# Kernel optimization log

Hardware: AMD Instinct MI355X
Metric: run time of the kernel (lower is better)

## Reference

```python
import jax, jax.numpy as jnp
import numpy as np

B, T, D, E, H = 4, 2048, 1024, 8, 1024  # H = hidden_units // num_experts


def setup_inputs() -> dict:
    key = jax.random.key(0)
    ks = jax.random.split(key, 5)
    s = 0.02
    return {
        "x": jax.random.normal(ks[0], (B, T, D), dtype=jnp.float32),
        "Wp": jax.random.normal(ks[1], (D, E), dtype=jnp.float32) * s,
        "bp": jnp.zeros((E,), dtype=jnp.float32),
        "W1": jax.random.normal(ks[2], (E, D, H), dtype=jnp.float32) * s,
        "b1": jnp.zeros((E, H), dtype=jnp.float32),
        "W2": jax.random.normal(ks[3], (E, H, D), dtype=jnp.float32) * s,
        "b2": jnp.zeros((E, D), dtype=jnp.float32),
    }


def reference(x, Wp, bp, W1, b1, W2, b2):
    b, t, d = x.shape
    e = Wp.shape[1]
    xf = x.reshape(-1, d)                       # [N, D]
    logits = xf @ Wp + bp                       # [N, E]
    probs = jax.nn.softmax(logits, axis=-1)     # [N, E]
    expert_chosen = jnp.argmax(probs, axis=-1)  # top-1 routing, [N]
    expert_probs = jnp.take_along_axis(probs, expert_chosen[:, None], axis=-1)  # [N,1]

    # Dense masked dispatch/combine (same math as gather-FFN-scatter; ReLU FFN,
    # dropout_rate=0 so dropout is identity).
    out = jnp.zeros_like(xf)
    for i in range(e):
        h = jax.nn.relu(xf @ W1[i] + b1[i])     # [N, H]
        y = h @ W2[i] + b2[i]                   # [N, D]
        mask = (expert_chosen == i).astype(xf.dtype)[:, None]
        out = out + mask * y

    # probs / probs.detach() == 1 in forward; gradient-routing trick preserved.
    out = out * (expert_probs / jax.lax.stop_gradient(expert_probs))
    return out.reshape(b, t, d), probs.reshape(b, t, e), expert_chosen.reshape(b, t)
```

## Files before the change

kernel.cpp:

```cpp
#include <hip/hip_runtime.h>
#include <stdint.h>

#define N_TOK 8192
#define D_DIM 1024
#define E_NUM 8

typedef float f32x4 __attribute__((ext_vector_type(4)));
typedef __bf16 bf16x8 __attribute__((ext_vector_type(8)));

__device__ __forceinline__ unsigned short f32_to_bf16_bits(float f) {
  union { float f; uint32_t u; } v; v.f = f;
  uint32_t u = v.u;
  uint32_t r = u + 0x7fffu + ((u >> 16) & 1u);
  return (unsigned short)(r >> 16);
}

__device__ __forceinline__ void load_lds16(const void* g, void* l) {
  __builtin_amdgcn_global_load_lds(
      (const __attribute__((address_space(1))) void*)g,
      (__attribute__((address_space(3))) void*)l, 16, 0, 0);
}

__device__ __forceinline__ void transpose_tile(unsigned short (*T)[72],
                                               const float* __restrict__ S,
                                               unsigned short* __restrict__ O,
                                               int r0, int c0, int t) {
  const int rr = t >> 4;
  const int cc = (t & 15) * 4;
#pragma unroll
  for (int p = 0; p < 4; p++) {
    int r = p * 16 + rr;
    float4 v = *reinterpret_cast<const float4*>(S + (size_t)(r0 + r) * 1024 + c0 + cc);
    T[cc + 0][r] = f32_to_bf16_bits(v.x);
    T[cc + 1][r] = f32_to_bf16_bits(v.y);
    T[cc + 2][r] = f32_to_bf16_bits(v.z);
    T[cc + 3][r] = f32_to_bf16_bits(v.w);
  }
  __syncthreads();
#pragma unroll
  for (int p = 0; p < 4; p++) {
    int c = p * 16 + rr;
    ushort4 o = *reinterpret_cast<const ushort4*>(&T[c][cc]);
    *reinterpret_cast<ushort4*>(O + (size_t)(c0 + c) * 1024 + r0 + cc) = o;
  }
}

__global__ __launch_bounds__(256) void wpt_kernel(const float* __restrict__ Wp,
                                                  float* __restrict__ WpT) {
  int i = blockIdx.x * 256 + threadIdx.x;
  int e = i >> 10, d = i & 1023;
  WpT[i] = Wp[(size_t)d * E_NUM + e];
}

__global__ __launch_bounds__(256) void routing_w1t_kernel(
    const float* __restrict__ x, const float* __restrict__ WpT,
    const float* __restrict__ bp, float* __restrict__ probs_out,
    float* __restrict__ chosenF, int* __restrict__ chosen,
    unsigned short* __restrict__ xb,
    const float* __restrict__ W1, unsigned short* __restrict__ W1t) {
  __shared__ __align__(16) unsigned short T[64][72];
  __shared__ __align__(16) float pbuf[4][8];
  if (blockIdx.x >= 2048) {
    const int tb = blockIdx.x - 2048;
    const int e = tb >> 8, rc = tb & 255;
    transpose_tile(T, W1 + ((size_t)e << 20), W1t + ((size_t)e << 20),
                   (rc >> 4) * 64, (rc & 15) * 64, threadIdx.x);
    return;
  }
  const int wave = threadIdx.x >> 6;
  const int lane = threadIdx.x & 63;
  const int token = blockIdx.x * 4 + wave;
  const float* xr = x + (size_t)token * D_DIM;
  unsigned short* xbr = xb + (size_t)token * D_DIM;
  double acc[E_NUM];
#pragma unroll
  for (int e = 0; e < E_NUM; e++) acc[e] = 0.0;
#pragma unroll
  for (int it = 0; it < 4; it++) {
    const int d0 = it * 256 + lane * 4;
    float4 xv = *reinterpret_cast<const float4*>(xr + d0);
    ushort4 o;
    o.x = f32_to_bf16_bits(xv.x);
    o.y = f32_to_bf16_bits(xv.y);
    o.z = f32_to_bf16_bits(xv.z);
    o.w = f32_to_bf16_bits(xv.w);
    *reinterpret_cast<ushort4*>(xbr + d0) = o;
#pragma unroll
    for (int e = 0; e < E_NUM; e++) {
      float4 w = *reinterpret_cast<const float4*>(WpT + (e << 10) + d0);
      acc[e] += (double)xv.x * (double)w.x;
      acc[e] += (double)xv.y * (double)w.y;
      acc[e] += (double)xv.z * (double)w.z;
      acc[e] += (double)xv.w * (double)w.w;
    }
  }
#pragma unroll
  for (int e = 0; e < E_NUM; e++) {
#pragma unroll
    for (int off = 32; off > 0; off >>= 1) acc[e] += __shfl_xor(acc[e], off);
  }
  if (lane == 0) {
    double lg[E_NUM];
#pragma unroll
    for (int e = 0; e < E_NUM; e++) lg[e] = acc[e] + (double)bp[e];
    int best = 0;
    double bv = lg[0];
#pragma unroll
    for (int e = 1; e < E_NUM; e++)
      if (lg[e] > bv) { bv = lg[e]; best = e; }
    double s = 0.0, ex[E_NUM];
#pragma unroll
    for (int e = 0; e < E_NUM; e++) { ex[e] = exp(lg[e] - bv); s += ex[e]; }
    double inv = 1.0 / s;
#pragma unroll
    for (int e = 0; e < E_NUM; e++) pbuf[wave][e] = (float)(ex[e] * inv);
    chosenF[token] = (float)best;
    chosen[token] = best;
  }
  __syncthreads();
  if (threadIdx.x < 8) {
    float4 v = *reinterpret_cast<const float4*>(
        &pbuf[threadIdx.x >> 1][(threadIdx.x & 1) * 4]);
    reinterpret_cast<float4*>(probs_out + (size_t)blockIdx.x * 32)[threadIdx.x] = v;
  }
}

__global__ __launch_bounds__(1024) void scan_scatter_kernel(
    const int* __restrict__ chosen, int* __restrict__ offsets,
    int* __restrict__ perm) {
  __shared__ int hist[E_NUM];
  __shared__ int curs[E_NUM];
  const int t = threadIdx.x;
  if (t < E_NUM) hist[t] = 0;
  __syncthreads();
  for (int n = t; n < N_TOK; n += 1024) atomicAdd(&hist[chosen[n]], 1);
  __syncthreads();
  if (t == 0) {
    int off = 0;
    for (int e = 0; e < E_NUM; e++) { offsets[e] = off; curs[e] = off; off += hist[e]; }
    offsets[E_NUM] = off;
  }
  __syncthreads();
  for (int n = t; n < N_TOK; n += 1024) {
    int e = chosen[n];
    int p = atomicAdd(&curs[e], 1);
    perm[p] = n;
  }
}

__global__ __launch_bounds__(256) void transpose_cast_kernel(
    const float* __restrict__ src, unsigned short* __restrict__ dst) {
  __shared__ __align__(16) unsigned short T[64][72];
  const int e = blockIdx.z;
  transpose_tile(T, src + ((size_t)e << 20), dst + ((size_t)e << 20),
                 blockIdx.y * 64, blockIdx.x * 64, threadIdx.x);
}

template <int MODE>
__global__ __launch_bounds__(256) void moe_gemm_kernel(
    const unsigned short* __restrict__ Abase,
    const unsigned short* __restrict__ Wt,
    const float* __restrict__ bias,
    const int* __restrict__ offsets, const int* __restrict__ perm,
    unsigned short* __restrict__ hb, float* __restrict__ out,
    const float* __restrict__ tsrc, unsigned short* __restrict__ tdst,
    int gemm_blocks) {
  __shared__ __align__(16) unsigned short As[128 * 64];
  __shared__ __align__(16) unsigned short Bs[64 * 64];

  if ((int)blockIdx.x >= gemm_blocks) {
    const int tb = blockIdx.x - gemm_blocks;
    const int e = tb >> 8, rc = tb & 255;
    auto T = reinterpret_cast<unsigned short(*)[72]>(As);
    transpose_tile(T, tsrc + ((size_t)e << 20), tdst + ((size_t)e << 20),
                   (rc >> 4) * 64, (rc & 15) * 64, threadIdx.x);
    return;
  }

  const int e = blockIdx.x & 7;
  const int slot = blockIdx.x >> 3;
  const int g0 = offsets[e];
  const int m_count = offsets[e + 1] - g0;
  const int m0 = (slot >> 4) * 128;
  if (m0 >= m_count) return;
  const int n0 = (slot & 15) * 64;

  const int tid = threadIdx.x;
  const int wid = tid >> 6, lane = tid & 63;
  const int lrow = lane >> 3;
  const int lchunk = lane & 7;

  const unsigned short* ga[4];
  const unsigned short* gb[2];
  unsigned short* la[4];
  unsigned short* lb[2];
  const unsigned short* WtE = Wt + ((size_t)e << 20);
#pragma unroll
  for (int t = 0; t < 4; t++) {
    const int rbase = t * 32 + wid * 8;
    const int r = rbase + lrow;
    int gr = g0 + m0 + r;
    if (gr > N_TOK - 1) gr = N_TOK - 1;
    const int arow = (MODE == 0) ? perm[gr] : gr;
    ga[t] = Abase + (size_t)arow * 1024 + lchunk * 8;
    la[t] = &As[rbase * 64];
  }
#pragma unroll
  for (int t = 0; t < 2; t++) {
    const int rbase = t * 32 + wid * 8;
    const int r = rbase + lrow;
    gb[t] = WtE + (size_t)(n0 + r) * 1024 + lchunk * 8;
    lb[t] = &Bs[rbase * 64];
  }

  f32x4 acc[4][2];
  const f32x4 zero4 = {0.f, 0.f, 0.f, 0.f};
#pragma unroll
  for (int i = 0; i < 4; i++)
#pragma unroll
    for (int j = 0; j < 2; j++) acc[i][j] = zero4;

  const int wr = wid >> 1, wc = wid & 1;
  const int lr = lane & 15, lk = lane >> 4;

  auto stage = [&]() {
#pragma unroll
    for (int t = 0; t < 4; t++) {
      load_lds16(ga[t], la[t]);
      ga[t] += 64;
    }
#pragma unroll
    for (int t = 0; t < 2; t++) {
      load_lds16(gb[t], lb[t]);
      gb[t] += 64;
    }
  };
  auto compute = [&]() {
#pragma unroll
    for (int kk = 0; kk < 64; kk += 32) {
      bf16x8 af[4], bfr[2];
#pragma unroll
      for (int mf = 0; mf < 4; mf++)
        af[mf] = *reinterpret_cast<const bf16x8*>(
            &As[(wr * 64 + mf * 16 + lr) * 64 + kk + lk * 8]);
#pragma unroll
      for (int nf = 0; nf < 2; nf++)
        bfr[nf] = *reinterpret_cast<const bf16x8*>(
            &Bs[(wc * 32 + nf * 16 + lr) * 64 + kk + lk * 8]);
#pragma unroll
      for (int mf = 0; mf < 4; mf++)
#pragma unroll
        for (int nf = 0; nf < 2; nf++)
          acc[mf][nf] = __builtin_amdgcn_mfma_f32_16x16x32_bf16(
              af[mf], bfr[nf], acc[mf][nf], 0, 0, 0);
    }
  };

  stage();
  __syncthreads();
  for (int kt = 0; kt < 16; kt++) {
    compute();
    if (kt < 15) {
      __syncthreads();
      stage();
      __syncthreads();
    }
  }

  const int mlim = m_count - m0;
#pragma unroll
  for (int nf = 0; nf < 2; nf++) {
    const int c = n0 + wc * 32 + nf * 16 + lr;
    const float bval = bias[(e << 10) + c];
#pragma unroll
    for (int mf = 0; mf < 4; mf++) {
#pragma unroll
      for (int j = 0; j < 4; j++) {
        const int lrow2 = wr * 64 + mf * 16 + lk * 4 + j;
        if (lrow2 < mlim) {
          float v = acc[mf][nf][j] + bval;
          if (MODE == 0) {
            v = v > 0.f ? v : 0.f;
            hb[(size_t)(g0 + m0 + lrow2) * 1024 + c] = f32_to_bf16_bits(v);
          } else {
            int token = perm[g0 + m0 + lrow2];
            out[(size_t)token * 1024 + c] = v;
          }
        }
      }
    }
  }
}

extern "C" void kernel_launch(void* const* d_in, const int* in_sizes, int n_in,
                              void* d_out, int out_size, void* d_ws, size_t ws_size,
                              hipStream_t stream) {
  const float* x = (const float*)d_in[0];
  const float* Wp = (const float*)d_in[1];
  const float* bp = (const float*)d_in[2];
  const float* W1 = (const float*)d_in[3];
  const float* b1 = (const float*)d_in[4];
  const float* W2 = (const float*)d_in[5];
  const float* b2 = (const float*)d_in[6];

  float* out = (float*)d_out;
  float* probs = out + (size_t)N_TOK * D_DIM;
  float* chosenF = probs + (size_t)N_TOK * E_NUM;

  char* ws = (char*)d_ws;
  int* chosen = (int*)(ws + 0);
  int* perm = (int*)(ws + 32768);
  float* WpT = (float*)(ws + 65536);
  int* offsets = (int*)(ws + 98304);
  const size_t MB16 = 16777216;
  unsigned short* xb = (unsigned short*)(ws + 131072);
  unsigned short* Wt1 = (unsigned short*)(ws + 131072 + MB16);
  const bool overlap = ws_size >= 131072 + 4 * MB16;
  unsigned short* Wt2 = (unsigned short*)(ws + 131072 + (overlap ? 2 : 1) * MB16);
  unsigned short* hb = (unsigned short*)(ws + 131072 + (overlap ? 3 : 2) * MB16);

  const int GEMM_BLOCKS = E_NUM * 64 * 16;

  wpt_kernel<<<32, 256, 0, stream>>>(Wp, WpT);
  routing_w1t_kernel<<<4096, 256, 0, stream>>>(x, WpT, bp, probs, chosenF, chosen,
                                               xb, W1, Wt1);
  scan_scatter_kernel<<<1, 1024, 0, stream>>>(chosen, offsets, perm);
  if (overlap) {
    moe_gemm_kernel<0><<<GEMM_BLOCKS + 2048, 256, 0, stream>>>(
        xb, Wt1, b1, offsets, perm, hb, nullptr, W2, Wt2, GEMM_BLOCKS);
  } else {
    moe_gemm_kernel<0><<<GEMM_BLOCKS, 256, 0, stream>>>(
        xb, Wt1, b1, offsets, perm, hb, nullptr, nullptr, nullptr, GEMM_BLOCKS);
    transpose_cast_kernel<<<dim3(16, 16, 8), 256, 0, stream>>>(W2, Wt2);
  }
  moe_gemm_kernel<1><<<GEMM_BLOCKS, 256, 0, stream>>>(
      hb, Wt2, b2, offsets, perm, nullptr, out, nullptr, nullptr, GEMM_BLOCKS);
}
```

Before: 129.8 us.

## Double-buffer LDS tiles and XOR-swizzle chunk layout in MoE GEMM

Splits the A and B shared-memory tiles into two buffers so the next K-tile's global-to-LDS loads are issued before computing on the current tile. This overlaps memory traffic with MFMA work and drops one barrier per iteration. It also XOR-swizzles the 16-byte chunk index by row, on both the global source and the fragment reads, to cut LDS bank conflicts. LDS use per block doubles, which may lower occupancy. The single remaining barrier relies on the async LDS loads having completed by the time it is reached.

```diff
diff --git a/kernel.cpp b/kernel.cpp
--- a/kernel.cpp
+++ b/kernel.cpp
@@ -165,13 +165,13 @@
     unsigned short* __restrict__ hb, float* __restrict__ out,
     const float* __restrict__ tsrc, unsigned short* __restrict__ tdst,
     int gemm_blocks) {
-  __shared__ __align__(16) unsigned short As[128 * 64];
-  __shared__ __align__(16) unsigned short Bs[64 * 64];
+  __shared__ __align__(16) unsigned short As[2][128 * 64];
+  __shared__ __align__(16) unsigned short Bs[2][64 * 64];
 
   if ((int)blockIdx.x >= gemm_blocks) {
     const int tb = blockIdx.x - gemm_blocks;
     const int e = tb >> 8, rc = tb & 255;
-    auto T = reinterpret_cast<unsigned short(*)[72]>(As);
+    auto T = reinterpret_cast<unsigned short(*)[72]>(&As[0][0]);
     transpose_tile(T, tsrc + ((size_t)e << 20), tdst + ((size_t)e << 20),
                    (rc >> 4) * 64, (rc & 15) * 64, threadIdx.x);
     return;
@@ -189,11 +189,11 @@
   const int wid = tid >> 6, lane = tid & 63;
   const int lrow = lane >> 3;
   const int lchunk = lane & 7;
+  const int schunk = lchunk ^ lrow;
 
   const unsigned short* ga[4];
   const unsigned short* gb[2];
-  unsigned short* la[4];
-  unsigned short* lb[2];
+  int abase[4], bbase[2];
   const unsigned short* WtE = Wt + ((size_t)e << 20);
 #pragma unroll
   for (int t = 0; t < 4; t++) {
@@ -202,15 +202,15 @@
     int gr = g0 + m0 + r;
     if (gr > N_TOK - 1) gr = N_TOK - 1;
     const int arow = (MODE == 0) ? perm[gr] : gr;
-    ga[t] = Abase + (size_t)arow * 1024 + lchunk * 8;
-    la[t] = &As[rbase * 64];
+    ga[t] = Abase + (size_t)arow * 1024 + schunk * 8;
+    abase[t] = rbase * 64;
   }
 #pragma unroll
   for (int t = 0; t < 2; t++) {
     const int rbase = t * 32 + wid * 8;
     const int r = rbase + lrow;
-    gb[t] = WtE + (size_t)(n0 + r) * 1024 + lchunk * 8;
-    lb[t] = &Bs[rbase * 64];
+    gb[t] = WtE + (size_t)(n0 + r) * 1024 + schunk * 8;
+    bbase[t] = rbase * 64;
   }
 
   f32x4 acc[4][2];
@@ -223,30 +223,34 @@
   const int wr = wid >> 1, wc = wid & 1;
   const int lr = lane & 15, lk = lane >> 4;
 
-  auto stage = [&]() {
+  auto stage = [&](int buf) {
 #pragma unroll
     for (int t = 0; t < 4; t++) {
-      load_lds16(ga[t], la[t]);
+      load_lds16(ga[t], &As[buf][abase[t]]);
       ga[t] += 64;
     }
 #pragma unroll
     for (int t = 0; t < 2; t++) {
-      load_lds16(gb[t], lb[t]);
+      load_lds16(gb[t], &Bs[buf][bbase[t]]);
       gb[t] += 64;
     }
   };
-  auto compute = [&]() {
+  auto compute = [&](int buf) {
 #pragma unroll
     for (int kk = 0; kk < 64; kk += 32) {
       bf16x8 af[4], bfr[2];
 #pragma unroll
-      for (int mf = 0; mf < 4; mf++)
-        af[mf] = *reinterpret_cast<const bf16x8*>(
-            &As[(wr * 64 + mf * 16 + lr) * 64 + kk + lk * 8]);
-#pragma unroll
-      for (int nf = 0; nf < 2; nf++)
-        bfr[nf] = *reinterpret_cast<const bf16x8*>(
-            &Bs[(wc * 32 + nf * 16 + lr) * 64 + kk + lk * 8]);
+      for (int mf = 0; mf < 4; mf++) {
+        const int ra = wr * 64 + mf * 16 + lr;
+        const int ca = ((kk >> 3) + lk) ^ (ra & 7);
+        af[mf] = *reinterpret_cast<const bf16x8*>(&As[buf][ra * 64 + ca * 8]);
+      }
+#pragma unroll
+      for (int nf = 0; nf < 2; nf++) {
+        const int rb = wc * 32 + nf * 16 + lr;
+        const int cb = ((kk >> 3) + lk) ^ (rb & 7);
+        bfr[nf] = *reinterpret_cast<const bf16x8*>(&Bs[buf][rb * 64 + cb * 8]);
+      }
 #pragma unroll
       for (int mf = 0; mf < 4; mf++)
 #pragma unroll
@@ -256,15 +260,14 @@
     }
   };
 
-  stage();
-  __syncthreads();
+  stage(0);
+  __syncthreads();
+  int cur = 0;
   for (int kt = 0; kt < 16; kt++) {
-    compute();
-    if (kt < 15) {
-      __syncthreads();
-      stage();
-      __syncthreads();
-    }
+    if (kt < 15) stage(cur ^ 1);
+    compute(cur);
+    if (kt < 15) __syncthreads();
+    cur ^= 1;
   }
 
   const int mlim = m_count - m0;
```

New measurement: 121.4 us. 1.07x faster.
